# Optimization experiments

Hardware: AMD Instinct MI355X
Metric: run time of the kernel (lower is better)

Reference implementation:

```python
import jax, jax.numpy as jnp
import numpy as np
from jax import lax

B, H, W, C = 8, 72, 72, 16
HID_E, HID_P, T = 128, 16, 64
P_EPS = 1e-06
ALIVE_TH = 0.1

# Sobel kernels. The torch code runs conv on NCHW with spatial dims (D2, D1)
# (x.transpose(1,3)); in our NHWC layout spatial dims are (D1, D2), so the
# equivalent kernel is the transpose. With angle=0: w1 = dx, w2 = dy = dx.T.
_DX = np.outer([1.0, 2.0, 1.0], [-1.0, 0.0, 1.0]) / 8.0
_W1_EFF = _DX.T            # transpose of w1
_W2_EFF = _DX              # transpose of w2 (= dy.T)


def _depthwise(x, k2d):
    c = x.shape[-1]
    ker = jnp.tile(jnp.asarray(k2d, x.dtype)[:, :, None, None], (1, 1, 1, c))  # HWIO (3,3,1,C)
    return lax.conv_general_dilated(x, ker, (1, 1), 'SAME',
                                    feature_group_count=c,
                                    dimension_numbers=('NHWC', 'HWIO', 'NHWC'))


def _conv2d(x, w, b):
    y = lax.conv_general_dilated(x, w, (1, 1), 'SAME',
                                 dimension_numbers=('NHWC', 'HWIO', 'NHWC'))
    return y + b


def _maxpool3(a):  # a: (B,H,W)
    return lax.reduce_window(a, -jnp.inf, lax.max, (1, 3, 3), (1, 1, 1),
                             [(0, 0), (1, 1), (1, 1)])


def setup_inputs() -> dict:
    key = jax.random.key(0)
    ks = jax.random.split(key, 6)
    c3 = 3 * C
    x = jax.random.uniform(ks[0], (B, H, W, C), jnp.float32)
    conv1_w = jax.random.normal(ks[1], (3, 3, c3, HID_P), jnp.float32) * (1.0 / np.sqrt(9 * c3))
    conv1_b = jnp.zeros((HID_P,), jnp.float32)
    conv2_w = jax.random.normal(ks[2], (3, 3, HID_P, 1), jnp.float32) * (1.0 / np.sqrt(9 * HID_P))
    conv2_b = jnp.zeros((1,), jnp.float32)
    fc0_w = jax.random.normal(ks[3], (c3, HID_E), jnp.float32) * (1.0 / np.sqrt(c3))
    fc0_b = jnp.zeros((HID_E,), jnp.float32)
    fc1_w = jax.random.normal(ks[4], (HID_E, C), jnp.float32) * 0.01  # torch init is zeros; small random for a non-degenerate baseline
    return dict(x=x, conv1_w=conv1_w, conv1_b=conv1_b, conv2_w=conv2_w,
                conv2_b=conv2_b, fc0_w=fc0_w, fc0_b=fc0_b, fc1_w=fc1_w)


def reference(x, conv1_w, conv1_b, conv2_w, conv2_b, fc0_w, fc0_b, fc1_w):
    base_key = jax.random.key(42)

    def perceive(x):  # (B,H,W,C) -> (B,H,W,3C)
        return jnp.concatenate([x, _depthwise(x, _W1_EFF), _depthwise(x, _W2_EFF)], axis=-1)

    def lambda_net(perc):  # (B,H,W,3C) -> (B,H,W)
        h = jax.nn.relu(_conv2d(perc, conv1_w, conv1_b))
        return jax.nn.sigmoid(_conv2d(h, conv2_w, conv2_b))[..., 0]

    def alive(x):  # alpha channel index 3
        return _maxpool3(x[..., 3]) > ALIVE_TH

    def update(x, lambdas, key):
        pre = alive(x)
        perc = perceive(x)
        dx = jax.nn.relu(perc @ fc0_w + fc0_b) @ fc1_w  # pointwise MLP, fc1 has no bias
        upd = 1.0 - jax.random.bernoulli(key, lambdas).astype(x.dtype)  # (B,H,W)
        xn = x + dx * upd[..., None]
        life = (pre & alive(xn)).astype(x.dtype)[..., None]
        return xn * life, upd, perc

    # initial perceive/lambda/update (step 0)
    perc0 = perceive(x)
    lam0 = lambda_net(perc0)
    x0, upd0, perc = update(x, lam0, jax.random.fold_in(base_key, 0))
    un0 = jnp.ones((x.shape[0], H, W), x.dtype)

    def step(carry, n):
        xc, updc, percc, un = carry
        lam = lambda_net(percc)
        p_n = un * lam + P_EPS
        out = (xc, p_n, lam, updc)
        un = un * (1.0 - lam)
        xn, updn, percn = update(xc, lam, jax.random.fold_in(base_key, n))
        return (xn, updn, percn, un), out

    _, (x_steps, p_steps, lam_steps, upd_steps) = lax.scan(
        step, (x0, upd0, perc, un0), jnp.arange(1, T + 1))
    p_norm = p_steps / jnp.sum(p_steps, axis=0)
    return x_steps, p_norm, lam_steps, upd_steps
```

## Files before the change

kernel.cpp:

```cpp
#include <hip/hip_runtime.h>
#include <cstdint>
#include <cmath>

#define B_    8
#define H_    72
#define W_    72
#define C_    16
#define C3_   48
#define HP_   16
#define HE_   128
#define T_    64
#define NCELL 41472

#define IBLK  648
#define NEDGE 2272
#define EBLK  36
#define S0STR 49

__host__ __device__ __forceinline__ void threefry2x32(uint32_t k0, uint32_t k1,
                                                      uint32_t& x0, uint32_t& x1) {
  uint32_t ks2 = k0 ^ k1 ^ 0x1BD11BDAu;
  x0 += k0; x1 += k1;
#define TF_R(r) { x0 += x1; x1 = (x1 << (r)) | (x1 >> (32 - (r))); x1 ^= x0; }
  TF_R(13) TF_R(15) TF_R(26) TF_R(6)
  x0 += k1; x1 += ks2 + 1u;
  TF_R(17) TF_R(29) TF_R(16) TF_R(24)
  x0 += ks2; x1 += k0 + 2u;
  TF_R(13) TF_R(15) TF_R(26) TF_R(6)
  x0 += k0; x1 += k1 + 3u;
  TF_R(17) TF_R(29) TF_R(16) TF_R(24)
  x0 += k1; x1 += ks2 + 4u;
  TF_R(13) TF_R(15) TF_R(26) TF_R(6)
  x0 += ks2; x1 += k0 + 5u;
#undef TF_R
}

__global__ void k_init(const float* __restrict__ xin, double* __restrict__ xA,
                       double* __restrict__ un) {
  int idx = blockIdx.x * 256 + threadIdx.x;
  if (idx < NCELL * C_) xA[idx] = (double)xin[idx];
  if (idx < NCELL) un[idx] = 1.0;
}

__global__ void k_prep(const float* __restrict__ w1, const float* __restrict__ b1,
                       const float* __restrict__ f0w, const float* __restrict__ f0b,
                       const float* __restrict__ f1w, const float* __restrict__ w2,
                       double* __restrict__ weffd, double* __restrict__ b1d,
                       double* __restrict__ fc0t, double* __restrict__ fc1d,
                       double* __restrict__ w2d, double* __restrict__ f0bd) {
  int gid = blockIdx.x * 256 + threadIdx.x;
  const int stride = 26 * 256;
  for (int t = gid; t < 6400; t += stride) {
    int oc = t & 15;
    int c  = (t >> 4) & 15;
    int pos = t >> 8;
    int u = pos / 5, v = pos % 5;
    double acc = 0.0;
    for (int ei = 0; ei < 3; ei++) {
      int di = u - ei; if (di < 0 || di > 2) continue;
      for (int ej = 0; ej < 3; ej++) {
        int dj = v - ej; if (dj < 0 || dj > 2) continue;
        const float* wb = w1 + (size_t)((ei * 3 + ej) * C3_) * HP_ + oc;
        if (di == 1 && dj == 1) acc += (double)wb[c * HP_];
        double rf1 = (di == 0) ? -0.125 : (di == 2) ? 0.125 : 0.0;
        if (rf1 != 0.0) {
          double cf1 = (dj == 1) ? 2.0 : 1.0;
          acc += (double)wb[(C_ + c) * HP_] * (rf1 * cf1);
        }
        double cf2 = (dj == 0) ? -0.125 : (dj == 2) ? 0.125 : 0.0;
        if (cf2 != 0.0) {
          double rf2 = (di == 1) ? 2.0 : 1.0;
          acc += (double)wb[(2 * C_ + c) * HP_] * (cf2 * rf2);
        }
      }
    }
    weffd[t] = acc;
  }
  for (int t = gid; t < C3_ * HE_; t += stride) {
    int k = t >> 7, e = t & 127;
    fc0t[e * S0STR + k] = (double)f0w[k * HE_ + e];
  }
  for (int t = gid; t < HE_ * C_; t += stride) fc1d[t] = (double)f1w[t];
  for (int t = gid; t < 144; t += stride) w2d[t] = (double)w2[t];
  for (int t = gid; t < HE_; t += stride) f0bd[t] = (double)f0b[t];
  for (int t = gid; t < HP_; t += stride) b1d[t] = (double)b1[t];
}

__global__ void __launch_bounds__(256) k_conv1f(const double* __restrict__ x,
    const double* __restrict__ weffd, const double* __restrict__ b1d,
    const float* __restrict__ w1f, double* __restrict__ hbuf) {
  __shared__ double sw[6400];
  __shared__ double sb[HP_];
  for (int t = threadIdx.x; t < 6400; t += 256) sw[t] = weffd[t];
  if (threadIdx.x < HP_) sb[threadIdx.x] = b1d[threadIdx.x];
  __syncthreads();

  if (blockIdx.x < IBLK) {
    int idx = blockIdx.x * 256 + threadIdx.x;
    int q = idx & 3;
    int cell = idx >> 2;
    int j = cell % W_; int t2 = cell / W_; int i = t2 % H_; int b = t2 / H_;
    if (i == 0 || i == H_ - 1 || j == 0 || j == W_ - 1) return;
    double acc0 = sb[(q << 2) + 0], acc1 = sb[(q << 2) + 1];
    double acc2 = sb[(q << 2) + 2], acc3 = sb[(q << 2) + 3];
    for (int u = 0; u < 5; u++) {
      int ii = i + u - 2; if (ii < 0 || ii >= H_) continue;
      for (int v = 0; v < 5; v++) {
        int jj = j + v - 2; if (jj < 0 || jj >= W_) continue;
        const double* xp = x + ((size_t)((b * H_ + ii) * W_ + jj) << 4);
        const double* wpos = sw + (u * 5 + v) * 256 + (q << 2);
#pragma unroll
        for (int ic = 0; ic < 16; ic += 2) {
          double x0 = xp[ic], x1 = xp[ic + 1];
          const double* w4a = wpos + ic * 16;
          const double* w4b = w4a + 16;
          acc0 = fma(x0, w4a[0], acc0); acc1 = fma(x0, w4a[1], acc1);
          acc2 = fma(x0, w4a[2], acc2); acc3 = fma(x0, w4a[3], acc3);
          acc0 = fma(x1, w4b[0], acc0); acc1 = fma(x1, w4b[1], acc1);
          acc2 = fma(x1, w4b[2], acc2); acc3 = fma(x1, w4b[3], acc3);
        }
      }
    }
    double* hp = hbuf + ((size_t)cell << 4) + (q << 2);
    hp[0] = acc0 > 0.0 ? acc0 : 0.0;
    hp[1] = acc1 > 0.0 ? acc1 : 0.0;
    hp[2] = acc2 > 0.0 ? acc2 : 0.0;
    hp[3] = acc3 > 0.0 ? acc3 : 0.0;
  } else {
    int eidx = (blockIdx.x - IBLK) * 256 + threadIdx.x;
    if (eidx >= NEDGE * 4) return;
    int q = eidx & 3;
    int e = eidx >> 2;
    int b = e / 284, r = e % 284;
    int i, j;
    if (r < 72)       { i = 0;       j = r; }
    else if (r < 144) { i = H_ - 1;  j = r - 72; }
    else if (r < 214) { i = r - 143; j = 0; }
    else              { i = r - 213; j = W_ - 1; }
    int cell = (b * H_ + i) * W_ + j;
    double acc0 = sb[(q << 2) + 0], acc1 = sb[(q << 2) + 1];
    double acc2 = sb[(q << 2) + 2], acc3 = sb[(q << 2) + 3];
    for (int ei = 0; ei < 3; ei++) {
      int pi = i + ei - 1; if (pi < 0 || pi >= H_) continue;
      for (int ej = 0; ej < 3; ej++) {
        int pj = j + ej - 1; if (pj < 0 || pj >= W_) continue;
        const float* wb = w1f + (size_t)((ei * 3 + ej) * C3_) * HP_ + (q << 2);
        for (int c = 0; c < C_; c++) {
          double v[3][3];
#pragma unroll
          for (int a2 = 0; a2 < 3; a2++) {
#pragma unroll
            for (int b2i = 0; b2i < 3; b2i++) {
              int ii2 = pi + a2 - 1, jj2 = pj + b2i - 1;
              bool ok = (ii2 >= 0 && ii2 < H_ && jj2 >= 0 && jj2 < W_);
              v[a2][b2i] = ok ? x[(((size_t)((b * H_ + ii2) * W_ + jj2)) << 4) + c] : 0.0;
            }
          }
          double ctr = v[1][1];
          double dw1 = (-v[0][0] - 2.0 * v[0][1] - v[0][2] + v[2][0] + 2.0 * v[2][1] + v[2][2]) * 0.125;
          double dw2 = (-v[0][0] + v[0][2] - 2.0 * v[1][0] + 2.0 * v[1][2] - v[2][0] + v[2][2]) * 0.125;
          const float* w0 = wb + c * HP_;
          const float* wA = wb + (C_ + c) * HP_;
          const float* wB = wb + (2 * C_ + c) * HP_;
          acc0 += ctr * (double)w0[0] + dw1 * (double)wA[0] + dw2 * (double)wB[0];
          acc1 += ctr * (double)w0[1] + dw1 * (double)wA[1] + dw2 * (double)wB[1];
          acc2 += ctr * (double)w0[2] + dw1 * (double)wA[2] + dw2 * (double)wB[2];
          acc3 += ctr * (double)w0[3] + dw1 * (double)wA[3] + dw2 * (double)wB[3];
        }
      }
    }
    double* hp = hbuf + ((size_t)cell << 4) + (q << 2);
    hp[0] = acc0 > 0.0 ? acc0 : 0.0;
    hp[1] = acc1 > 0.0 ? acc1 : 0.0;
    hp[2] = acc2 > 0.0 ? acc2 : 0.0;
    hp[3] = acc3 > 0.0 ? acc3 : 0.0;
  }
}

__global__ void __launch_bounds__(256) k_upd(
    const double* __restrict__ x, const double* __restrict__ hbuf,
    const double* __restrict__ lamPrev, const double* __restrict__ fc0t,
    const double* __restrict__ fc1d, const double* __restrict__ w2d,
    const double* __restrict__ f0bd, const float* __restrict__ b2,
    double* __restrict__ lamNext, double* __restrict__ xn,
    float* __restrict__ out_upd, double* __restrict__ un,
    float* __restrict__ out_lam, double* __restrict__ p_buf,
    uint32_t k0, uint32_t k1, int n) {
  __shared__ double s0[HE_ * S0STR];
  __shared__ double sw2[144];
  __shared__ double sb0[HE_];
  for (int t = threadIdx.x; t < HE_ * S0STR; t += 256) {
    int e = t / S0STR, k = t - e * S0STR;
    s0[t] = (k < C3_) ? fc0t[t] : 0.0;
  }
  if (threadIdx.x < 144) sw2[threadIdx.x] = w2d[threadIdx.x];
  if (threadIdx.x < HE_) sb0[threadIdx.x] = f0bd[threadIdx.x];
  __syncthreads();
  int idx = blockIdx.x * 256 + threadIdx.x;
  int q = idx & 3;
  int cell = idx >> 2;
  int j = cell % W_; int t2 = cell / W_; int i = t2 % H_; int b = t2 / H_;

  double z = 0.0;
  for (int di = 0; di < 3; di++) {
    int ii = i + di - 1; if (ii < 0 || ii >= H_) continue;
    for (int dj = 0; dj < 3; dj++) {
      int jj = j + dj - 1; if (jj < 0 || jj >= W_) continue;
      const double* hh = hbuf + ((size_t)((b * H_ + ii) * W_ + jj) << 4) + (q << 2);
      const double* ww = sw2 + (di * 3 + dj) * HP_ + (q << 2);
      z = fma(hh[0], ww[0], z); z = fma(hh[1], ww[1], z);
      z = fma(hh[2], ww[2], z); z = fma(hh[3], ww[3], z);
    }
  }
  z += __shfl_xor(z, 1);
  z += __shfl_xor(z, 2);
  z += (double)b2[0];
  double lamF = 1.0 / (1.0 + exp(-z));
  if (q == 0) lamNext[cell] = lamF;
  double l = (n == 0) ? lamF : lamPrev[cell];

  if (n >= 1 && q == 0) {
    size_t o = (size_t)(n - 1) * NCELL + cell;
    out_lam[o] = (float)l;
    double u = un[cell];
    p_buf[o] = u * l + 1e-6;
    un[cell] = u * (1.0 - l);
  }

  uint32_t r0 = 0u, r1 = (uint32_t)cell;
  threefry2x32(k0, k1, r0, r1);
  double uf = (double)(r0 ^ r1) * 0x1p-32;
  double upd = (uf < l) ? 0.0 : 1.0;
  if (q == 0) out_upd[(size_t)n * NCELL + cell] = (float)upd;

  double pv[C3_];
#pragma unroll
  for (int k = 0; k < C3_; k++) pv[k] = 0.0;
#pragma unroll
  for (int p = 0; p < 9; p++) {
    const int di = p / 3, dj = p % 3;
    const double k1c = (di == 0 ? -0.125 : di == 2 ? 0.125 : 0.0) * (dj == 1 ? 2.0 : 1.0);
    const double k2c = (dj == 0 ? -0.125 : dj == 2 ? 0.125 : 0.0) * (di == 1 ? 2.0 : 1.0);
    int ii = i + di - 1, jj = j + dj - 1;
    if (ii < 0 || ii >= H_ || jj < 0 || jj >= W_) continue;
    const double* xp = x + ((size_t)((b * H_ + ii) * W_ + jj) << 4);
#pragma unroll
    for (int c = 0; c < C_; c++) {
      double xv = xp[c];
      if (p == 4) pv[c] += xv;
      if (k1c != 0.0) pv[C_ + c] = fma(k1c, xv, pv[C_ + c]);
      if (k2c != 0.0) pv[2 * C_ + c] = fma(k2c, xv, pv[2 * C_ + c]);
    }
  }

  double dx[C_];
#pragma unroll
  for (int c = 0; c < C_; c++) dx[c] = 0.0;
  for (int m = 0; m < 32; m += 2) {
    int e0 = (m << 2) + q;
    int e1 = e0 + 4;
    const double* w0 = s0 + e0 * S0STR;
    const double* w1r = s0 + e1 * S0STR;
    double a0 = sb0[e0], a1 = sb0[e1];
#pragma unroll
    for (int k = 0; k < C3_; k++) {
      a0 = fma(pv[k], w0[k], a0);
      a1 = fma(pv[k], w1r[k], a1);
    }
    a0 = a0 > 0.0 ? a0 : 0.0;
    a1 = a1 > 0.0 ? a1 : 0.0;
    const double* v0 = fc1d + (e0 << 4);
    const double* v1 = fc1d + (e1 << 4);
#pragma unroll
    for (int c = 0; c < C_; c++) {
      dx[c] = fma(a0, v0[c], dx[c]);
      dx[c] = fma(a1, v1[c], dx[c]);
    }
  }
#pragma unroll
  for (int c = 0; c < C_; c++) {
    dx[c] += __shfl_xor(dx[c], 1);
    dx[c] += __shfl_xor(dx[c], 2);
  }
  double d0 = (q & 2) ? ((q & 1) ? dx[12] : dx[8])  : ((q & 1) ? dx[4] : dx[0]);
  double d1 = (q & 2) ? ((q & 1) ? dx[13] : dx[9])  : ((q & 1) ? dx[5] : dx[1]);
  double d2 = (q & 2) ? ((q & 1) ? dx[14] : dx[10]) : ((q & 1) ? dx[6] : dx[2]);
  double d3 = (q & 2) ? ((q & 1) ? dx[15] : dx[11]) : ((q & 1) ? dx[7] : dx[3]);
  const double* xc = x + ((size_t)cell << 4) + (q << 2);
  double* xo = xn + ((size_t)cell << 4) + (q << 2);
  xo[0] = xc[0] + d0 * upd;
  xo[1] = xc[1] + d1 * upd;
  xo[2] = xc[2] + d2 * upd;
  xo[3] = xc[3] + d3 * upd;
}

__global__ void k_life(const double* __restrict__ xold, const double* __restrict__ xn,
                       double* __restrict__ xout, float* __restrict__ out_x, int n) {
  int idx = blockIdx.x * 256 + threadIdx.x;
  int c = idx & 15;
  int cell = idx >> 4;
  int j = cell % W_; int t = cell / W_; int i = t % H_; int b = t / H_;
  double mo = -1e300, mn2 = -1e300;
  for (int di = -1; di <= 1; di++) {
    int ii = i + di; if (ii < 0 || ii >= H_) continue;
    for (int dj = -1; dj <= 1; dj++) {
      int jj = j + dj; if (jj < 0 || jj >= W_) continue;
      size_t nb = (size_t)((b * H_ + ii) * W_ + jj) * C_;
      double a0 = xold[nb + 3]; if (a0 > mo) mo = a0;
      double a1 = xn[nb + 3];   if (a1 > mn2) mn2 = a1;
    }
  }
  bool life = (mo > 0.1) && (mn2 > 0.1);
  double v = life ? xn[((size_t)cell << 4) + c] : 0.0;
  xout[((size_t)cell << 4) + c] = v;
  out_x[(size_t)n * NCELL * C_ + ((size_t)cell << 4) + c] = (float)v;
}

__global__ void k_emit(const double* __restrict__ lam, const double* __restrict__ un,
                       float* __restrict__ out_lam, double* __restrict__ p_buf) {
  int cell = blockIdx.x * 256 + threadIdx.x;
  double l = lam[cell];
  size_t o = (size_t)(T_ - 1) * NCELL + cell;
  out_lam[o] = (float)l;
  p_buf[o] = un[cell] * l + 1e-6;
}

__global__ void k_pnorm(const double* __restrict__ p_buf, float* __restrict__ out_p) {
  int cell = blockIdx.x * 256 + threadIdx.x;
  double s = 0.0;
  for (int t = 0; t < T_; t++) s += p_buf[(size_t)t * NCELL + cell];
  for (int t = 0; t < T_; t++)
    out_p[(size_t)t * NCELL + cell] = (float)(p_buf[(size_t)t * NCELL + cell] / s);
}

extern "C" void kernel_launch(void* const* d_in, const int* in_sizes, int n_in,
                              void* d_out, int out_size, void* d_ws, size_t ws_size,
                              hipStream_t stream) {
  const float* xin = (const float*)d_in[0];
  const float* w1  = (const float*)d_in[1];
  const float* b1  = (const float*)d_in[2];
  const float* w2  = (const float*)d_in[3];
  const float* b2  = (const float*)d_in[4];
  const float* f0w = (const float*)d_in[5];
  const float* f0b = (const float*)d_in[6];
  const float* f1w = (const float*)d_in[7];

  float* out     = (float*)d_out;
  float* out_x   = out;
  float* out_p   = out_x + (size_t)T_ * NCELL * C_;
  float* out_lam = out_p + (size_t)T_ * NCELL;
  float* out_upd = out_lam + (size_t)T_ * NCELL;

  double* ws    = (double*)d_ws;
  double* xA    = ws;
  double* xB    = xA + (size_t)NCELL * C_;
  double* xn    = xB + (size_t)NCELL * C_;
  double* hbuf  = xn + (size_t)NCELL * C_;
  double* lamA  = hbuf + (size_t)NCELL * HP_;
  double* lamB  = lamA + NCELL;
  double* un    = lamB + NCELL;
  double* p_buf = un + NCELL;
  double* weffd = p_buf + (size_t)T_ * NCELL;
  double* fc0t  = weffd + 6400;
  double* fc1d  = fc0t + HE_ * S0STR;
  double* w2d   = fc1d + HE_ * C_;
  double* f0bd  = w2d + 144;
  double* b1d   = f0bd + HE_;

  k_init<<<2592, 256, 0, stream>>>(xin, xA, un);
  k_prep<<<26, 256, 0, stream>>>(w1, b1, f0w, f0b, f1w, w2,
                                 weffd, b1d, fc0t, fc1d, w2d, f0bd);

  double* cur = lamA;
  double* nxt = lamB;

  for (int n = 0; n <= T_ - 1; n++) {
    k_conv1f<<<IBLK + EBLK, 256, 0, stream>>>(xA, weffd, b1d, w1, hbuf);
    uint32_t kx0 = 0u, kx1 = (uint32_t)n;
    threefry2x32(0u, 42u, kx0, kx1);
    k_upd<<<IBLK, 256, 0, stream>>>(xA, hbuf, cur, fc0t, fc1d, w2d, f0bd, b2,
                                    (n == 0 ? cur : nxt), xn, out_upd, un,
                                    out_lam, p_buf, kx0, kx1, n);
    k_life<<<2592, 256, 0, stream>>>(xA, xn, xB, out_x, n);
    { double* t = xA; xA = xB; xB = t; }
    if (n >= 1) { double* t = cur; cur = nxt; nxt = t; }
  }

  k_emit<<<162, 256, 0, stream>>>(cur, un, out_lam, p_buf);
  k_pnorm<<<162, 256, 0, stream>>>(p_buf, out_p);
}
```

Measured before the change: 14.80 ms.

## Restructure conv1 and update kernels to wave-uniform weight access

Reassigns work so each wavefront handles 64 cells with the same output-channel or hidden-unit slice. Weight reads become wave-uniform global loads that can be scalarised, which drops the shared-memory weight staging. The conv1 interior computes 8 output channels per thread, and the edge path computes one channel per thread using pre-converted double weights. k_upd splits the 128 hidden units across two waves and reduces their partial results through shared memory, replacing the 4-lane shuffle reduction. This adds register pressure (48 perception values plus 16 dx accumulators per thread) and leaves one of the two waves idle for the lambda and update phase.

```diff
diff --git a/kernel.cpp b/kernel.cpp
--- a/kernel.cpp
+++ b/kernel.cpp
@@ -11,11 +11,7 @@
 #define HE_   128
 #define T_    64
 #define NCELL 41472
-
-#define IBLK  648
 #define NEDGE 2272
-#define EBLK  36
-#define S0STR 49
 
 __host__ __device__ __forceinline__ void threefry2x32(uint32_t k0, uint32_t k1,
                                                       uint32_t& x0, uint32_t& x1) {
@@ -47,7 +43,8 @@
                        const float* __restrict__ f1w, const float* __restrict__ w2,
                        double* __restrict__ weffd, double* __restrict__ b1d,
                        double* __restrict__ fc0t, double* __restrict__ fc1d,
-                       double* __restrict__ w2d, double* __restrict__ f0bd) {
+                       double* __restrict__ w2d, double* __restrict__ f0bd,
+                       double* __restrict__ w1d) {
   int gid = blockIdx.x * 256 + threadIdx.x;
   const int stride = 26 * 256;
   for (int t = gid; t < 6400; t += stride) {
@@ -78,73 +75,71 @@
   }
   for (int t = gid; t < C3_ * HE_; t += stride) {
     int k = t >> 7, e = t & 127;
-    fc0t[e * S0STR + k] = (double)f0w[k * HE_ + e];
+    fc0t[e * C3_ + k] = (double)f0w[t];
   }
   for (int t = gid; t < HE_ * C_; t += stride) fc1d[t] = (double)f1w[t];
   for (int t = gid; t < 144; t += stride) w2d[t] = (double)w2[t];
   for (int t = gid; t < HE_; t += stride) f0bd[t] = (double)f0b[t];
   for (int t = gid; t < HP_; t += stride) b1d[t] = (double)b1[t];
-}
-
-__global__ void __launch_bounds__(256) k_conv1f(const double* __restrict__ x,
+  for (int t = gid; t < 3 * 3 * C3_ * HP_; t += stride) w1d[t] = (double)w1[t];
+}
+
+__global__ void __launch_bounds__(256) k_conv1(const double* __restrict__ x,
     const double* __restrict__ weffd, const double* __restrict__ b1d,
-    const float* __restrict__ w1f, double* __restrict__ hbuf) {
-  __shared__ double sw[6400];
-  __shared__ double sb[HP_];
-  for (int t = threadIdx.x; t < 6400; t += 256) sw[t] = weffd[t];
-  if (threadIdx.x < HP_) sb[threadIdx.x] = b1d[threadIdx.x];
-  __syncthreads();
-
-  if (blockIdx.x < IBLK) {
-    int idx = blockIdx.x * 256 + threadIdx.x;
-    int q = idx & 3;
-    int cell = idx >> 2;
+    const double* __restrict__ w1d, double* __restrict__ hbuf) {
+  int lane = threadIdx.x & 63;
+  int wv = __builtin_amdgcn_readfirstlane(threadIdx.x >> 6);
+  if (blockIdx.x < 324) {
+    int gw = blockIdx.x * 4 + wv;
+    int cellw = gw >> 1;
+    int ocb = (gw & 1) << 3;
+    int cell = (cellw << 6) + lane;
     int j = cell % W_; int t2 = cell / W_; int i = t2 % H_; int b = t2 / H_;
     if (i == 0 || i == H_ - 1 || j == 0 || j == W_ - 1) return;
-    double acc0 = sb[(q << 2) + 0], acc1 = sb[(q << 2) + 1];
-    double acc2 = sb[(q << 2) + 2], acc3 = sb[(q << 2) + 3];
+    double acc[8];
+#pragma unroll
+    for (int o = 0; o < 8; o++) acc[o] = b1d[ocb + o];
+#pragma unroll 1
     for (int u = 0; u < 5; u++) {
       int ii = i + u - 2; if (ii < 0 || ii >= H_) continue;
+#pragma unroll 1
       for (int v = 0; v < 5; v++) {
         int jj = j + v - 2; if (jj < 0 || jj >= W_) continue;
         const double* xp = x + ((size_t)((b * H_ + ii) * W_ + jj) << 4);
-        const double* wpos = sw + (u * 5 + v) * 256 + (q << 2);
-#pragma unroll
-        for (int ic = 0; ic < 16; ic += 2) {
-          double x0 = xp[ic], x1 = xp[ic + 1];
-          const double* w4a = wpos + ic * 16;
-          const double* w4b = w4a + 16;
-          acc0 = fma(x0, w4a[0], acc0); acc1 = fma(x0, w4a[1], acc1);
-          acc2 = fma(x0, w4a[2], acc2); acc3 = fma(x0, w4a[3], acc3);
-          acc0 = fma(x1, w4b[0], acc0); acc1 = fma(x1, w4b[1], acc1);
-          acc2 = fma(x1, w4b[2], acc2); acc3 = fma(x1, w4b[3], acc3);
+        const double* wp = weffd + (u * 5 + v) * 256 + ocb;
+        double xv[16];
+#pragma unroll
+        for (int ic = 0; ic < 16; ic++) xv[ic] = xp[ic];
+#pragma unroll
+        for (int ic = 0; ic < 16; ic++) {
+#pragma unroll
+          for (int o = 0; o < 8; o++)
+            acc[o] = fma(xv[ic], wp[ic * 16 + o], acc[o]);
         }
       }
     }
-    double* hp = hbuf + ((size_t)cell << 4) + (q << 2);
-    hp[0] = acc0 > 0.0 ? acc0 : 0.0;
-    hp[1] = acc1 > 0.0 ? acc1 : 0.0;
-    hp[2] = acc2 > 0.0 ? acc2 : 0.0;
-    hp[3] = acc3 > 0.0 ? acc3 : 0.0;
+    double* hp = hbuf + ((size_t)cell << 4) + ocb;
+#pragma unroll
+    for (int o = 0; o < 8; o++) hp[o] = acc[o] > 0.0 ? acc[o] : 0.0;
   } else {
-    int eidx = (blockIdx.x - IBLK) * 256 + threadIdx.x;
-    if (eidx >= NEDGE * 4) return;
-    int q = eidx & 3;
-    int e = eidx >> 2;
-    int b = e / 284, r = e % 284;
+    int gw = (blockIdx.x - 324) * 4 + wv;
+    int oc = gw & 15;
+    int grp = gw >> 4;
+    int ecell = (grp << 6) + lane;
+    if (ecell >= NEDGE) return;
+    int b = ecell / 284, r = ecell % 284;
     int i, j;
     if (r < 72)       { i = 0;       j = r; }
     else if (r < 144) { i = H_ - 1;  j = r - 72; }
     else if (r < 214) { i = r - 143; j = 0; }
     else              { i = r - 213; j = W_ - 1; }
     int cell = (b * H_ + i) * W_ + j;
-    double acc0 = sb[(q << 2) + 0], acc1 = sb[(q << 2) + 1];
-    double acc2 = sb[(q << 2) + 2], acc3 = sb[(q << 2) + 3];
+    double acc = b1d[oc];
     for (int ei = 0; ei < 3; ei++) {
       int pi = i + ei - 1; if (pi < 0 || pi >= H_) continue;
       for (int ej = 0; ej < 3; ej++) {
         int pj = j + ej - 1; if (pj < 0 || pj >= W_) continue;
-        const float* wb = w1f + (size_t)((ei * 3 + ej) * C3_) * HP_ + (q << 2);
+        const double* wb = w1d + (size_t)((ei * 3 + ej) * C3_) * HP_ + oc;
         for (int c = 0; c < C_; c++) {
           double v[3][3];
 #pragma unroll
@@ -159,25 +154,15 @@
           double ctr = v[1][1];
           double dw1 = (-v[0][0] - 2.0 * v[0][1] - v[0][2] + v[2][0] + 2.0 * v[2][1] + v[2][2]) * 0.125;
           double dw2 = (-v[0][0] + v[0][2] - 2.0 * v[1][0] + 2.0 * v[1][2] - v[2][0] + v[2][2]) * 0.125;
-          const float* w0 = wb + c * HP_;
-          const float* wA = wb + (C_ + c) * HP_;
-          const float* wB = wb + (2 * C_ + c) * HP_;
-          acc0 += ctr * (double)w0[0] + dw1 * (double)wA[0] + dw2 * (double)wB[0];
-          acc1 += ctr * (double)w0[1] + dw1 * (double)wA[1] + dw2 * (double)wB[1];
-          acc2 += ctr * (double)w0[2] + dw1 * (double)wA[2] + dw2 * (double)wB[2];
-          acc3 += ctr * (double)w0[3] + dw1 * (double)wA[3] + dw2 * (double)wB[3];
+          acc += ctr * wb[c * HP_] + dw1 * wb[(C_ + c) * HP_] + dw2 * wb[(2 * C_ + c) * HP_];
         }
       }
     }
-    double* hp = hbuf + ((size_t)cell << 4) + (q << 2);
-    hp[0] = acc0 > 0.0 ? acc0 : 0.0;
-    hp[1] = acc1 > 0.0 ? acc1 : 0.0;
-    hp[2] = acc2 > 0.0 ? acc2 : 0.0;
-    hp[3] = acc3 > 0.0 ? acc3 : 0.0;
-  }
-}
-
-__global__ void __launch_bounds__(256) k_upd(
+    hbuf[((size_t)cell << 4) + oc] = acc > 0.0 ? acc : 0.0;
+  }
+}
+
+__global__ void __launch_bounds__(128) k_upd(
     const double* __restrict__ x, const double* __restrict__ hbuf,
     const double* __restrict__ lamPrev, const double* __restrict__ fc0t,
     const double* __restrict__ fc1d, const double* __restrict__ w2d,
@@ -186,52 +171,11 @@
     float* __restrict__ out_upd, double* __restrict__ un,
     float* __restrict__ out_lam, double* __restrict__ p_buf,
     uint32_t k0, uint32_t k1, int n) {
-  __shared__ double s0[HE_ * S0STR];
-  __shared__ double sw2[144];
-  __shared__ double sb0[HE_];
-  for (int t = threadIdx.x; t < HE_ * S0STR; t += 256) {
-    int e = t / S0STR, k = t - e * S0STR;
-    s0[t] = (k < C3_) ? fc0t[t] : 0.0;
-  }
-  if (threadIdx.x < 144) sw2[threadIdx.x] = w2d[threadIdx.x];
-  if (threadIdx.x < HE_) sb0[threadIdx.x] = f0bd[threadIdx.x];
-  __syncthreads();
-  int idx = blockIdx.x * 256 + threadIdx.x;
-  int q = idx & 3;
-  int cell = idx >> 2;
+  __shared__ double sdx[64][17];
+  int lane = threadIdx.x & 63;
+  int wv = __builtin_amdgcn_readfirstlane(threadIdx.x >> 6);
+  int cell = (blockIdx.x << 6) + lane;
   int j = cell % W_; int t2 = cell / W_; int i = t2 % H_; int b = t2 / H_;
-
-  double z = 0.0;
-  for (int di = 0; di < 3; di++) {
-    int ii = i + di - 1; if (ii < 0 || ii >= H_) continue;
-    for (int dj = 0; dj < 3; dj++) {
-      int jj = j + dj - 1; if (jj < 0 || jj >= W_) continue;
-      const double* hh = hbuf + ((size_t)((b * H_ + ii) * W_ + jj) << 4) + (q << 2);
-      const double* ww = sw2 + (di * 3 + dj) * HP_ + (q << 2);
-      z = fma(hh[0], ww[0], z); z = fma(hh[1], ww[1], z);
-      z = fma(hh[2], ww[2], z); z = fma(hh[3], ww[3], z);
-    }
-  }
-  z += __shfl_xor(z, 1);
-  z += __shfl_xor(z, 2);
-  z += (double)b2[0];
-  double lamF = 1.0 / (1.0 + exp(-z));
-  if (q == 0) lamNext[cell] = lamF;
-  double l = (n == 0) ? lamF : lamPrev[cell];
-
-  if (n >= 1 && q == 0) {
-    size_t o = (size_t)(n - 1) * NCELL + cell;
-    out_lam[o] = (float)l;
-    double u = un[cell];
-    p_buf[o] = u * l + 1e-6;
-    un[cell] = u * (1.0 - l);
-  }
-
-  uint32_t r0 = 0u, r1 = (uint32_t)cell;
-  threefry2x32(k0, k1, r0, r1);
-  double uf = (double)(r0 ^ r1) * 0x1p-32;
-  double upd = (uf < l) ? 0.0 : 1.0;
-  if (q == 0) out_upd[(size_t)n * NCELL + cell] = (float)upd;
 
   double pv[C3_];
 #pragma unroll
@@ -256,42 +200,78 @@
   double dx[C_];
 #pragma unroll
   for (int c = 0; c < C_; c++) dx[c] = 0.0;
-  for (int m = 0; m < 32; m += 2) {
-    int e0 = (m << 2) + q;
-    int e1 = e0 + 4;
-    const double* w0 = s0 + e0 * S0STR;
-    const double* w1r = s0 + e1 * S0STR;
-    double a0 = sb0[e0], a1 = sb0[e1];
+  int ebase = wv << 6;
+#pragma unroll 2
+  for (int eg = 0; eg < 64; eg += 4) {
+    const double* wrow = fc0t + (size_t)(ebase + eg) * C3_;
+    double a0 = f0bd[ebase + eg + 0];
+    double a1 = f0bd[ebase + eg + 1];
+    double a2 = f0bd[ebase + eg + 2];
+    double a3 = f0bd[ebase + eg + 3];
 #pragma unroll
     for (int k = 0; k < C3_; k++) {
-      a0 = fma(pv[k], w0[k], a0);
-      a1 = fma(pv[k], w1r[k], a1);
+      a0 = fma(pv[k], wrow[k], a0);
+      a1 = fma(pv[k], wrow[C3_ + k], a1);
+      a2 = fma(pv[k], wrow[2 * C3_ + k], a2);
+      a3 = fma(pv[k], wrow[3 * C3_ + k], a3);
     }
     a0 = a0 > 0.0 ? a0 : 0.0;
     a1 = a1 > 0.0 ? a1 : 0.0;
-    const double* v0 = fc1d + (e0 << 4);
-    const double* v1 = fc1d + (e1 << 4);
+    a2 = a2 > 0.0 ? a2 : 0.0;
+    a3 = a3 > 0.0 ? a3 : 0.0;
+    const double* v0 = fc1d + ((size_t)(ebase + eg) << 4);
 #pragma unroll
     for (int c = 0; c < C_; c++) {
-      dx[c] = fma(a0, v0[c], dx[c]);
-      dx[c] = fma(a1, v1[c], dx[c]);
-    }
-  }
-#pragma unroll
-  for (int c = 0; c < C_; c++) {
-    dx[c] += __shfl_xor(dx[c], 1);
-    dx[c] += __shfl_xor(dx[c], 2);
-  }
-  double d0 = (q & 2) ? ((q & 1) ? dx[12] : dx[8])  : ((q & 1) ? dx[4] : dx[0]);
-  double d1 = (q & 2) ? ((q & 1) ? dx[13] : dx[9])  : ((q & 1) ? dx[5] : dx[1]);
-  double d2 = (q & 2) ? ((q & 1) ? dx[14] : dx[10]) : ((q & 1) ? dx[6] : dx[2]);
-  double d3 = (q & 2) ? ((q & 1) ? dx[15] : dx[11]) : ((q & 1) ? dx[7] : dx[3]);
-  const double* xc = x + ((size_t)cell << 4) + (q << 2);
-  double* xo = xn + ((size_t)cell << 4) + (q << 2);
-  xo[0] = xc[0] + d0 * upd;
-  xo[1] = xc[1] + d1 * upd;
-  xo[2] = xc[2] + d2 * upd;
-  xo[3] = xc[3] + d3 * upd;
+      double s = fma(a0, v0[c], dx[c]);
+      s = fma(a1, v0[16 + c], s);
+      s = fma(a2, v0[32 + c], s);
+      s = fma(a3, v0[48 + c], s);
+      dx[c] = s;
+    }
+  }
+
+  if (wv == 1) {
+#pragma unroll
+    for (int c = 0; c < C_; c++) sdx[lane][c] = dx[c];
+  }
+  __syncthreads();
+  if (wv == 1) return;
+
+#pragma unroll
+  for (int c = 0; c < C_; c++) dx[c] += sdx[lane][c];
+
+  double z = (double)b2[0];
+  for (int di = 0; di < 3; di++) {
+    int ii = i + di - 1; if (ii < 0 || ii >= H_) continue;
+    for (int dj = 0; dj < 3; dj++) {
+      int jj = j + dj - 1; if (jj < 0 || jj >= W_) continue;
+      const double* hh = hbuf + ((size_t)((b * H_ + ii) * W_ + jj) << 4);
+      const double* ww = w2d + (di * 3 + dj) * HP_;
+#pragma unroll
+      for (int ic = 0; ic < HP_; ic++) z = fma(hh[ic], ww[ic], z);
+    }
+  }
+  double lamF = 1.0 / (1.0 + exp(-z));
+  lamNext[cell] = lamF;
+  double l = (n == 0) ? lamF : lamPrev[cell];
+
+  if (n >= 1) {
+    size_t o = (size_t)(n - 1) * NCELL + cell;
+    out_lam[o] = (float)l;
+    double u = un[cell];
+    p_buf[o] = u * l + 1e-6;
+    un[cell] = u * (1.0 - l);
+  }
+
+  uint32_t r0 = 0u, r1 = (uint32_t)cell;
+  threefry2x32(k0, k1, r0, r1);
+  double uf = (double)(r0 ^ r1) * 0x1p-32;
+  double upd = (uf < l) ? 0.0 : 1.0;
+  out_upd[(size_t)n * NCELL + cell] = (float)upd;
+  const double* xc = x + ((size_t)cell << 4);
+  double* xo = xn + ((size_t)cell << 4);
+#pragma unroll
+  for (int c = 0; c < C_; c++) xo[c] = xc[c] + dx[c] * upd;
 }
 
 __global__ void k_life(const double* __restrict__ xold, const double* __restrict__ xn,
@@ -362,25 +342,26 @@
   double* p_buf = un + NCELL;
   double* weffd = p_buf + (size_t)T_ * NCELL;
   double* fc0t  = weffd + 6400;
-  double* fc1d  = fc0t + HE_ * S0STR;
+  double* fc1d  = fc0t + HE_ * C3_;
   double* w2d   = fc1d + HE_ * C_;
   double* f0bd  = w2d + 144;
   double* b1d   = f0bd + HE_;
+  double* w1d   = b1d + HP_;
 
   k_init<<<2592, 256, 0, stream>>>(xin, xA, un);
   k_prep<<<26, 256, 0, stream>>>(w1, b1, f0w, f0b, f1w, w2,
-                                 weffd, b1d, fc0t, fc1d, w2d, f0bd);
+                                 weffd, b1d, fc0t, fc1d, w2d, f0bd, w1d);
 
   double* cur = lamA;
   double* nxt = lamB;
 
   for (int n = 0; n <= T_ - 1; n++) {
-    k_conv1f<<<IBLK + EBLK, 256, 0, stream>>>(xA, weffd, b1d, w1, hbuf);
+    k_conv1<<<468, 256, 0, stream>>>(xA, weffd, b1d, w1d, hbuf);
     uint32_t kx0 = 0u, kx1 = (uint32_t)n;
     threefry2x32(0u, 42u, kx0, kx1);
-    k_upd<<<IBLK, 256, 0, stream>>>(xA, hbuf, cur, fc0t, fc1d, w2d, f0bd, b2,
-                                    (n == 0 ? cur : nxt), xn, out_upd, un,
-                                    out_lam, p_buf, kx0, kx1, n);
+    k_upd<<<648, 128, 0, stream>>>(xA, hbuf, cur, fc0t, fc1d, w2d, f0bd, b2,
+                                   (n == 0 ? cur : nxt), xn, out_upd, un,
+                                   out_lam, p_buf, kx0, kx1, n);
     k_life<<<2592, 256, 0, stream>>>(xA, xn, xB, out_x, n);
     { double* t = xA; xA = xB; xB = t; }
     if (n >= 1) { double* t = cur; cur = nxt; nxt = t; }
```

After: 14.78 ms. About the same (-0.1%).
